# Optimization experiments

Measured on AMD Instinct MI355X. Metric: run time of the kernel, lower is better.

## Reference

```python
import jax, jax.numpy as jnp
import numpy as np

HEADS = 8
GROUPS = 32   # Group_cnt in the source
WIN = 16      # config.local_window_size


def _gn_nc(x, groups, eps):
    # group_norm on [N, C] (affine=False)
    N, C = x.shape
    xg = x.reshape(N, groups, C // groups)
    m = xg.mean(axis=2, keepdims=True)
    v = xg.var(axis=2, keepdims=True)
    return ((xg - m) / jnp.sqrt(v + eps)).reshape(N, C)


def _gn_nchw(x, groups, eps):
    # group_norm on [B, C, H, W] (affine=False)
    B, C, H, W = x.shape
    xg = x.reshape(B, groups, C // groups, H, W)
    m = xg.mean(axis=(2, 3, 4), keepdims=True)
    v = xg.var(axis=(2, 3, 4), keepdims=True)
    return ((xg - m) / jnp.sqrt(v + eps)).reshape(B, C, H, W)


def _conv3x3(x, w, b=None):
    y = jax.lax.conv_general_dilated(x, w, (1, 1), 'SAME',
                                     dimension_numbers=('NCHW', 'OIHW', 'NCHW'))
    return y if b is None else y + b[None, :, None, None]


def _forward(x, temb, conv1_w, conv1_b, conv2_w, g_diff, g_res, g2, g3,
             qkv2_w, qkv2_b, out2_w, qkv3_w, qkv3_b, out3_w,
             lsa_qkv_w, lsa_out_w):
    # ---- Residual_Block (layer1) ----
    h = _gn_nchw(x, GROUPS, 1e-6)
    h = _conv3x3(h, conv1_w, conv1_b)
    h = h + g_diff * temb[:, :, None, None]      # gate_diffusion (ReZero-style gate)
    h = jax.nn.silu(h)
    h = _gn_nchw(h, GROUPS, 1e-6)
    h = _conv3x3(h, conv2_w)
    h = _gn_nchw(h, GROUPS, 1e-6)
    x = x + g_res * h                            # gate_residual

    B, C, Fq, T = x.shape
    Dh = C // HEADS
    scale = 1.0 / jnp.sqrt(jnp.float32(Dh))      # (F/heads)**0.5 divisor

    # ---- SelfAttention over frequency axis (layer2): batch B*T, seq Fq ----
    xf = x.transpose(0, 3, 2, 1).reshape(B * T, Fq, C)
    qkv = xf @ qkv2_w + qkv2_b                   # [B*T, Fq, 3C]
    q, k, v = [t.reshape(B * T, Fq, HEADS, Dh) for t in jnp.split(qkv, 3, axis=-1)]
    p = jax.nn.softmax(jnp.einsum('bLhf,blhf->bLlh', q, k) * scale, axis=2)
    y = jnp.einsum('blhf,bLlh->bLhf', v, p).reshape(B * T, Fq, C) @ out2_w
    y = _gn_nc(y.reshape(-1, C), GROUPS, 1e-5).reshape(B * T, Fq, C)
    xf = xf + g2 * y                             # gate2

    # ---- GlobalAttention over time axis (layer3): batch B*Fq, seq T ----
    xt = xf.reshape(B, T, Fq, C).transpose(0, 2, 1, 3).reshape(B * Fq, T, C)
    qkv = xt @ qkv3_w + qkv3_b
    q, k, v = [t.reshape(B * Fq, T, HEADS, Dh) for t in jnp.split(qkv, 3, axis=-1)]
    p = jax.nn.softmax(jnp.einsum('bhf,blhf->blh', q.mean(axis=1), k) * scale, axis=1)
    y = jnp.einsum('blhf,blh->bhf', v, p).reshape(B * Fq, C) @ out3_w
    y = _gn_nc(y, GROUPS, 1e-5).reshape(B * Fq, 1, C)
    xt = xt + g3 * y                             # gate3, broadcast over T
    x = xt.reshape(B, Fq, T, C).transpose(0, 3, 1, 2)

    # ---- LSA_block (layer4): pre-norm local windowed attention along T, residual ----
    h = _gn_nchw(x, GROUPS, 1e-5)
    h = h.transpose(0, 2, 3, 1).reshape(B * Fq, T, C)
    nw = T // WIN
    qkv = (h @ lsa_qkv_w).reshape(B * Fq, nw, WIN, 3 * C)
    q, k, v = [t.reshape(B * Fq, nw, WIN, HEADS, Dh) for t in jnp.split(qkv, 3, axis=-1)]
    p = jax.nn.softmax(jnp.einsum('nwqhd,nwkhd->nwqkh', q, k) * scale, axis=3)
    o = jnp.einsum('nwqkh,nwkhd->nwqhd', p, v).reshape(B * Fq, T, C) @ lsa_out_w
    return x + o.reshape(B, Fq, T, C).transpose(0, 3, 1, 2)


def setup_inputs() -> dict:
    key = jax.random.key(0)
    ks = jax.random.split(key, 10)
    B, C, Fq, T = 4, 256, 64, 256
    w = lambda k, s: jax.random.normal(k, s, dtype=jnp.float32) * 0.02
    return {
        'x': jax.random.normal(ks[0], (B, C, Fq, T), dtype=jnp.float32),
        'temb': jax.random.normal(ks[1], (B, C), dtype=jnp.float32),
        'conv1_w': w(ks[2], (C, C, 3, 3)),
        'conv1_b': jnp.zeros((C,), jnp.float32),
        'conv2_w': w(ks[3], (C, C, 3, 3)),
        'g_diff': jnp.full((1,), 0.5, jnp.float32),
        'g_res': jnp.full((1,), 0.5, jnp.float32),
        'g2': jnp.full((1,), 0.5, jnp.float32),
        'g3': jnp.full((1,), 0.5, jnp.float32),
        'qkv2_w': w(ks[4], (C, 3 * C)),
        'qkv2_b': jnp.zeros((3 * C,), jnp.float32),
        'out2_w': w(ks[5], (C, C)),
        'qkv3_w': w(ks[6], (C, 3 * C)),
        'qkv3_b': jnp.zeros((3 * C,), jnp.float32),
        'out3_w': w(ks[7], (C, C)),
        'lsa_qkv_w': w(ks[8], (C, 3 * C)),
        'lsa_out_w': w(ks[9], (C, C)),
    }


def reference(x, temb, conv1_w, conv1_b, conv2_w, g_diff, g_res, g2, g3,
              qkv2_w, qkv2_b, out2_w, qkv3_w, qkv3_b, out3_w,
              lsa_qkv_w, lsa_out_w):
    return _forward(x, temb, conv1_w, conv1_b, conv2_w, g_diff, g_res, g2, g3,
                    qkv2_w, qkv2_b, out2_w, qkv3_w, qkv3_b, out3_w,
                    lsa_qkv_w, lsa_out_w)
```

## Files before the change

### kernel.cpp

```cpp
#include <hip/hip_runtime.h>

#define NN 16777216
#define CC 256
#define FF 64
#define TT 256

typedef short v8s __attribute__((ext_vector_type(8)));
typedef float v4f __attribute__((ext_vector_type(4)));

__device__ __forceinline__ unsigned short f2bf(float f) {
  unsigned u = __float_as_uint(f);
  u += 0x7fff + ((u >> 16) & 1);
  return (unsigned short)(u >> 16);
}
__device__ __forceinline__ float bf2f(unsigned short h) {
  return __uint_as_float(((unsigned)h) << 16);
}
__device__ __forceinline__ unsigned packbf2(float a, float b) {
  return (unsigned)f2bf(a) | ((unsigned)f2bf(b) << 16);
}
__device__ __forceinline__ void unpack8(uint4 u, float* d) {
  d[0] = __uint_as_float(u.x << 16); d[1] = __uint_as_float(u.x & 0xffff0000u);
  d[2] = __uint_as_float(u.y << 16); d[3] = __uint_as_float(u.y & 0xffff0000u);
  d[4] = __uint_as_float(u.z << 16); d[5] = __uint_as_float(u.z & 0xffff0000u);
  d[6] = __uint_as_float(u.w << 16); d[7] = __uint_as_float(u.w & 0xffff0000u);
}

__device__ __forceinline__ void blockReduce2(float& a, float& b, float* sbuf) {
  #pragma unroll
  for (int off = 32; off > 0; off >>= 1) {
    a += __shfl_down(a, off, 64);
    b += __shfl_down(b, off, 64);
  }
  int w = threadIdx.x >> 6;
  if ((threadIdx.x & 63) == 0) { sbuf[w] = a; sbuf[4 + w] = b; }
  __syncthreads();
  if (threadIdx.x == 0) {
    a = sbuf[0] + sbuf[1] + sbuf[2] + sbuf[3];
    b = sbuf[4] + sbuf[5] + sbuf[6] + sbuf[7];
  }
}

__global__ void prep_all_k(const float* __restrict__ c1w, const float* __restrict__ c2w,
    const float* __restrict__ q2w, const float* __restrict__ o2w, const float* __restrict__ q3w,
    const float* __restrict__ lqw, const float* __restrict__ low,
    unsigned short* __restrict__ WB1, unsigned short* __restrict__ WB2,
    unsigned short* __restrict__ Q2T, unsigned short* __restrict__ O2T,
    unsigned short* __restrict__ Q3T, unsigned short* __restrict__ LQT,
    unsigned short* __restrict__ LOT, float* __restrict__ stats) {
  long s = (long)blockIdx.x * 256 + threadIdx.x;
  if (s < 1024) { stats[s] = 0.f; return; }
  s -= 1024;
  if (s < 589824) {
    int co = (int)(s / 2304), r = (int)(s % 2304);
    int ci = r / 9, tap = r % 9;
    WB1[(tap * 256 + co) * 256 + ci] = f2bf(c1w[s]);
    return;
  }
  s -= 589824;
  if (s < 589824) {
    int co = (int)(s / 2304), r = (int)(s % 2304);
    int ci = r / 9, tap = r % 9;
    WB2[(tap * 256 + co) * 256 + ci] = f2bf(c2w[s]);
    return;
  }
  s -= 589824;
  if (s < 196608) { int k = (int)(s / 768), n = (int)(s % 768); Q2T[n * 256 + k] = f2bf(q2w[s]); return; }
  s -= 196608;
  if (s < 65536)  { int k = (int)(s / 256), n = (int)(s % 256); O2T[n * 256 + k] = f2bf(o2w[s]); return; }
  s -= 65536;
  if (s < 196608) { int k = (int)(s / 768), n = (int)(s % 768); Q3T[n * 256 + k] = f2bf(q3w[s]); return; }
  s -= 196608;
  if (s < 196608) { int k = (int)(s / 768), n = (int)(s % 768); LQT[n * 256 + k] = f2bf(lqw[s]); return; }
  s -= 196608;
  if (s < 65536)  { int k = (int)(s / 256), n = (int)(s % 256); LOT[n * 256 + k] = f2bf(low[s]); return; }
}

__global__ __launch_bounds__(256) void gn_stats_contig(const float* __restrict__ src, float* __restrict__ stats) {
  __shared__ float sbuf[8];
  int grp = blockIdx.x >> 3, chunk = blockIdx.x & 7;
  const float4* p = (const float4*)src + grp * 32768 + chunk * 4096;
  float s = 0.f, ss = 0.f;
  for (int i = threadIdx.x; i < 4096; i += 256) {
    float4 v = p[i];
    s += v.x + v.y + v.z + v.w;
    ss += v.x * v.x + v.y * v.y + v.z * v.z + v.w * v.w;
  }
  blockReduce2(s, ss, sbuf);
  if (threadIdx.x == 0) { atomicAdd(&stats[grp], s); atomicAdd(&stats[128 + grp], ss); }
}

__global__ __launch_bounds__(256) void gn_apply_tr_k(const float* __restrict__ src,
    const float* __restrict__ stats, unsigned short* __restrict__ XC, float eps) {
  __shared__ float sT[32][33];
  int bx = blockIdx.x;
  int r = bx >> 6;
  int c0 = ((bx >> 3) & 7) * 32;
  int t0 = (bx & 7) * 32;
  int b = r >> 6, f = r & 63;
  int tl = threadIdx.x & 31, tr = threadIdx.x >> 5;
  #pragma unroll
  for (int i = 0; i < 4; ++i) {
    int c = c0 + tr + i * 8;
    int grp = b * 32 + (c >> 3);
    float mean = stats[grp] * (1.f / 131072.f);
    float var = stats[128 + grp] * (1.f / 131072.f) - mean * mean;
    float rv = rsqrtf(var + eps);
    float v = src[((b * 256 + c) * 64 + f) * 256 + t0 + tl];
    sT[tr + i * 8][tl] = (v - mean) * rv;
  }
  __syncthreads();
  #pragma unroll
  for (int i = 0; i < 4; ++i) {
    int t = t0 + tr + i * 8;
    XC[(((size_t)(b * 64 + f)) * 256 + t) * 256 + c0 + tl] = f2bf(sT[tl][tr + i * 8]);
  }
}

__global__ __launch_bounds__(256) void gn_tr_resid_k(const float* __restrict__ h,
    const float* __restrict__ x, const float* __restrict__ stats,
    const float* __restrict__ gate, float* __restrict__ XF, float eps) {
  __shared__ float sT[32][33];
  int bx = blockIdx.x;
  int r = bx >> 6;
  int c0 = ((bx >> 3) & 7) * 32;
  int t0 = (bx & 7) * 32;
  int b = r >> 6, f = r & 63;
  int tl = threadIdx.x & 31, tr = threadIdx.x >> 5;
  float g = gate[0];
  #pragma unroll
  for (int i = 0; i < 4; ++i) {
    int c = c0 + tr + i * 8;
    int grp = b * 32 + (c >> 3);
    float mean = stats[grp] * (1.f / 131072.f);
    float var = stats[128 + grp] * (1.f / 131072.f) - mean * mean;
    float rv = rsqrtf(var + eps);
    int idx = ((b * 256 + c) * 64 + f) * 256 + t0 + tl;
    sT[tr + i * 8][tl] = x[idx] + g * (h[idx] - mean) * rv;
  }
  __syncthreads();
  #pragma unroll
  for (int i = 0; i < 4; ++i) {
    int t = t0 + tr + i * 8;
    XF[(((size_t)(b * 256 + t)) * 64 + f) * 256 + c0 + tl] = sT[tl][tr + i * 8];
  }
}

__global__ __launch_bounds__(256, 4) void conv3x3_mfma_k(const unsigned short* __restrict__ XC,
    const unsigned short* __restrict__ wb, const float* __restrict__ bias,
    const float* __restrict__ temb, const float* __restrict__ gd,
    float* __restrict__ out, float* __restrict__ ostats, int mode) {
  __shared__ __align__(16) unsigned short sIn[258][40];
  __shared__ __align__(16) unsigned short sW[3][64][40];
  int bid0 = blockIdx.y * 64 + blockIdx.x;
  int nb = (bid0 & 7) * 128 + (bid0 >> 3);
  int f  = nb & 63;
  int yy = nb >> 6;
  int b  = yy >> 2;
  int co0 = (yy & 3) * 64;
  int tid = threadIdx.x;
  int wave = tid >> 6, lane = tid & 63;
  int lm = lane & 15, quad = lane >> 4;
  int w64 = wave * 64;
  v4f acc[4][4];
  #pragma unroll
  for (int i = 0; i < 4; ++i)
    #pragma unroll
    for (int j = 0; j < 4; ++j) acc[i][j] = (v4f)(0.f);

  for (int ci0 = 0; ci0 < 256; ci0 += 32) {
    for (int df = 0; df < 3; ++df) {
      __syncthreads();
      for (int s = tid; s < 1032; s += 256) {
        int tl = s >> 2, part = s & 3;
        int fi = f + df - 1, tg = tl - 1;
        uint4 val = make_uint4(0, 0, 0, 0);
        if (fi >= 0 && fi < 64 && tg >= 0 && tg < 256)
          val = *(const uint4*)&XC[(((size_t)(b * 64 + fi)) * 256 + tg) * 256 + ci0 + part * 8];
        *(uint4*)&sIn[tl][part * 8] = val;
      }
      for (int s = tid; s < 768; s += 256) {
        int tap3 = s >> 8, r = s & 255;
        int co = r >> 2, part = r & 3;
        *(uint4*)&sW[tap3][co][part * 8] =
            *(const uint4*)&wb[((size_t)((df * 3 + tap3) * 256) + co0 + co) * 256 + ci0 + part * 8];
      }
      __syncthreads();
      #pragma unroll
      for (int dt = 0; dt < 3; ++dt) {
        v8s A[4];
        #pragma unroll
        for (int mt = 0; mt < 4; ++mt)
          A[mt] = *(const v8s*)&sIn[w64 + mt * 16 + lm + dt][quad * 8];
        #pragma unroll
        for (int nt = 0; nt < 4; ++nt) {
          v8s B = *(const v8s*)&sW[dt][nt * 16 + lm][quad * 8];
          #pragma unroll
          for (int mt = 0; mt < 4; ++mt)
            acc[mt][nt] = __builtin_amdgcn_mfma_f32_16x16x32_bf16(A[mt], B, acc[mt][nt], 0, 0, 0);
        }
      }
    }
  }
  __syncthreads();
  float* sStat = (float*)sIn;
  float gdv = mode ? gd[0] : 0.f;
  float sch, qch;
  #pragma unroll
  for (int nt = 0; nt < 4; ++nt) {
    int co = co0 + nt * 16 + lm;
    float bb = 0.f;
    if (mode) bb = bias[co] + gdv * temb[b * 256 + co];
    sch = 0.f; qch = 0.f;
    #pragma unroll
    for (int mt = 0; mt < 4; ++mt) {
      int t = w64 + mt * 16 + quad * 4;
      float v0 = acc[mt][nt][0] + bb, v1 = acc[mt][nt][1] + bb;
      float v2 = acc[mt][nt][2] + bb, v3 = acc[mt][nt][3] + bb;
      if (mode) {
        v0 = v0 / (1.f + expf(-v0)); v1 = v1 / (1.f + expf(-v1));
        v2 = v2 / (1.f + expf(-v2)); v3 = v3 / (1.f + expf(-v3));
      }
      float4 o; o.x = v0; o.y = v1; o.z = v2; o.w = v3;
      *(float4*)&out[(((size_t)b * 256 + co) * 64 + f) * 256 + t] = o;
      sch += v0 + v1 + v2 + v3;
      qch += v0 * v0 + v1 * v1 + v2 * v2 + v3 * v3;
    }
    sch += __shfl_xor(sch, 16); qch += __shfl_xor(qch, 16);
    sch += __shfl_xor(sch, 32); qch += __shfl_xor(qch, 32);
    if (quad == 0) {
      sStat[((wave * 4 + nt) * 16 + lm) * 2]     = sch;
      sStat[((wave * 4 + nt) * 16 + lm) * 2 + 1] = qch;
    }
  }
  __syncthreads();
  if (tid < 64) {
    int c = tid;
    int nt = c >> 4, lmm = c & 15;
    float s = 0.f, q = 0.f;
    #pragma unroll
    for (int w = 0; w < 4; ++w) {
      s += sStat[((w * 4 + nt) * 16 + lmm) * 2];
      q += sStat[((w * 4 + nt) * 16 + lmm) * 2 + 1];
    }
    s += __shfl_xor(s, 1); q += __shfl_xor(q, 1);
    s += __shfl_xor(s, 2); q += __shfl_xor(q, 2);
    s += __shfl_xor(s, 4); q += __shfl_xor(q, 4);
    if ((c & 7) == 0) {
      int g = (co0 + c) >> 3;
      atomicAdd(&ostats[b * 32 + g], s);
      atomicAdd(&ostats[128 + b * 32 + g], q);
    }
  }
}

__global__ __launch_bounds__(256) void gemm_af32_k(const float* __restrict__ A, int lda,
    const unsigned short* __restrict__ BT, const float* __restrict__ bias,
    unsigned short* __restrict__ Cb, int ldc,
    const float* __restrict__ gstats, int growbase, float eps) {
  __shared__ __align__(16) unsigned short sA[128][40];
  __shared__ __align__(16) unsigned short sB[128][40];
  int nbx = gridDim.x;
  int nwg = nbx * gridDim.y;
  int bid0 = blockIdx.y * nbx + blockIdx.x;
  int nb = (bid0 & 7) * (nwg >> 3) + (bid0 >> 3);
  int n0 = (nb % nbx) * 128, m0 = (nb / nbx) * 128;
  int tid = threadIdx.x;
  int wave = tid >> 6, lane = tid & 63;
  int wm = wave >> 1, wn = wave & 1;
  int lm = lane & 15, quad = lane >> 4;
  v4f acc[4][4];
  #pragma unroll
  for (int i = 0; i < 4; ++i)
    #pragma unroll
    for (int j = 0; j < 4; ++j) acc[i][j] = (v4f)(0.f);

  for (int k0 = 0; k0 < 256; k0 += 32) {
    __syncthreads();
    #pragma unroll
    for (int i = 0; i < 4; ++i) {
      int s = tid + i * 256;
      int row = s >> 3, k4 = s & 7;
      float4 av = *(const float4*)&A[(size_t)(m0 + row) * lda + k0 + k4 * 4];
      if (gstats) {
        int grp = ((growbase + m0 + row) >> 14) * 32 + ((k0 + k4 * 4) >> 3);
        float mean = gstats[grp] * (1.f / 131072.f);
        float var = gstats[128 + grp] * (1.f / 131072.f) - mean * mean;
        float rr = rsqrtf(var + eps);
        av.x = (av.x - mean) * rr; av.y = (av.y - mean) * rr;
        av.z = (av.z - mean) * rr; av.w = (av.w - mean) * rr;
      }
      *(uint2*)&sA[row][k4 * 4] = make_uint2(packbf2(av.x, av.y), packbf2(av.z, av.w));
    }
    #pragma unroll
    for (int i = 0; i < 2; ++i) {
      int s = tid + i * 256;
      int n = s >> 2, part = s & 3;
      *(uint4*)&sB[n][part * 8] = *(const uint4*)&BT[(size_t)(n0 + n) * 256 + k0 + part * 8];
    }
    __syncthreads();
    v8s Af[4];
    #pragma unroll
    for (int mt = 0; mt < 4; ++mt)
      Af[mt] = *(const v8s*)&sA[wm * 64 + mt * 16 + lm][quad * 8];
    #pragma unroll
    for (int nt = 0; nt < 4; ++nt) {
      v8s Bf = *(const v8s*)&sB[wn * 64 + nt * 16 + lm][quad * 8];
      #pragma unroll
      for (int mt = 0; mt < 4; ++mt)
        acc[mt][nt] = __builtin_amdgcn_mfma_f32_16x16x32_bf16(Af[mt], Bf, acc[mt][nt], 0, 0, 0);
    }
  }
  #pragma unroll
  for (int nt = 0; nt < 4; ++nt) {
    int col = n0 + wn * 64 + nt * 16 + lm;
    float bb = bias ? bias[col] : 0.f;
    #pragma unroll
    for (int mt = 0; mt < 4; ++mt) {
      int row = m0 + wm * 64 + mt * 16 + quad * 4;
      #pragma unroll
      for (int r = 0; r < 4; ++r)
        Cb[(size_t)(row + r) * ldc + col] = f2bf(acc[mt][nt][r] + bb);
    }
  }
}

__global__ __launch_bounds__(256) void gemm_abf16_k(const unsigned short* __restrict__ A, int lda,
    const unsigned short* __restrict__ BT, float* __restrict__ xf,
    unsigned short* __restrict__ Cb, int ldc, const float* __restrict__ gate) {
  __shared__ __align__(16) unsigned short sA[128][40];
  __shared__ __align__(16) unsigned short sB[128][40];
  int nbx = gridDim.x;
  int nwg = nbx * gridDim.y;
  int bid0 = blockIdx.y * nbx + blockIdx.x;
  int nb = (bid0 & 7) * (nwg >> 3) + (bid0 >> 3);
  int n0 = (nb % nbx) * 128, m0 = (nb / nbx) * 128;
  int tid = threadIdx.x;
  int wave = tid >> 6, lane = tid & 63;
  int wm = wave >> 1, wn = wave & 1;
  int lm = lane & 15, quad = lane >> 4;
  v4f acc[4][4];
  #pragma unroll
  for (int i = 0; i < 4; ++i)
    #pragma unroll
    for (int j = 0; j < 4; ++j) acc[i][j] = (v4f)(0.f);

  for (int k0 = 0; k0 < 256; k0 += 32) {
    __syncthreads();
    #pragma unroll
    for (int i = 0; i < 2; ++i) {
      int s = tid + i * 256;
      int row = s >> 2, part = s & 3;
      *(uint4*)&sA[row][part * 8] = *(const uint4*)&A[(size_t)(m0 + row) * lda + k0 + part * 8];
      *(uint4*)&sB[row][part * 8] = *(const uint4*)&BT[(size_t)(n0 + row) * 256 + k0 + part * 8];
    }
    __syncthreads();
    v8s Af[4];
    #pragma unroll
    for (int mt = 0; mt < 4; ++mt)
      Af[mt] = *(const v8s*)&sA[wm * 64 + mt * 16 + lm][quad * 8];
    #pragma unroll
    for (int nt = 0; nt < 4; ++nt) {
      v8s Bf = *(const v8s*)&sB[wn * 64 + nt * 16 + lm][quad * 8];
      #pragma unroll
      for (int mt = 0; mt < 4; ++mt)
        acc[mt][nt] = __builtin_amdgcn_mfma_f32_16x16x32_bf16(Af[mt], Bf, acc[mt][nt], 0, 0, 0);
    }
  }
  if (xf) {
    float g = gate[0];
    #pragma unroll
    for (int mt = 0; mt < 4; ++mt) {
      int rowb = m0 + wm * 64 + mt * 16 + quad * 4;
      #pragma unroll
      for (int r = 0; r < 4; ++r) {
        #pragma unroll
        for (int nt = 0; nt < 4; ++nt) {
          float v = acc[mt][nt][r];
          float s = v, q = v * v;
          s += __shfl_xor(s, 1); q += __shfl_xor(q, 1);
          s += __shfl_xor(s, 2); q += __shfl_xor(q, 2);
          s += __shfl_xor(s, 4); q += __shfl_xor(q, 4);
          float m = s * 0.125f;
          float var = q * 0.125f - m * m;
          float norm = (v - m) * rsqrtf(var + 1e-5f);
          int col = n0 + wn * 64 + nt * 16 + lm;
          size_t idx = (size_t)(rowb + r) * 256 + col;
          xf[idx] += g * norm;
        }
      }
    }
  } else {
    #pragma unroll
    for (int nt = 0; nt < 4; ++nt) {
      int col = n0 + wn * 64 + nt * 16 + lm;
      #pragma unroll
      for (int mt = 0; mt < 4; ++mt) {
        int row = m0 + wm * 64 + mt * 16 + quad * 4;
        #pragma unroll
        for (int r = 0; r < 4; ++r)
          Cb[(size_t)(row + r) * ldc + col] = f2bf(acc[mt][nt][r]);
      }
    }
  }
}

__global__ __launch_bounds__(256) void gemm_k(const float* __restrict__ A, int lda,
    const float* __restrict__ Bm, int N, const float* __restrict__ bias,
    float* __restrict__ Cm, int ldc, int gn) {
  __shared__ __align__(16) float sA[16][64];
  __shared__ __align__(16) float sB[16][64];
  int n0 = blockIdx.x * 64, m0 = blockIdx.y * 64;
  int tid = threadIdx.x;
  int tx = tid & 15, ty = tid >> 4;
  int arow = m0 + (tid >> 2), acol = (tid & 3) * 4;
  int brow = tid >> 4, bcol = (tid & 15) * 4;
  float acc[4][4] = {};
  for (int k0 = 0; k0 < 256; k0 += 16) {
    __syncthreads();
    float4 av = *(const float4*)&A[(size_t)arow * lda + k0 + acol];
    sA[acol + 0][tid >> 2] = av.x;
    sA[acol + 1][tid >> 2] = av.y;
    sA[acol + 2][tid >> 2] = av.z;
    sA[acol + 3][tid >> 2] = av.w;
    *(float4*)&sB[brow][bcol] = *(const float4*)&Bm[(k0 + brow) * N + n0 + bcol];
    __syncthreads();
    #pragma unroll
    for (int kk = 0; kk < 16; ++kk) {
      float4 a = *(const float4*)&sA[kk][ty * 4];
      float4 b = *(const float4*)&sB[kk][tx * 4];
      float aa[4] = {a.x, a.y, a.z, a.w};
      float bb[4] = {b.x, b.y, b.z, b.w};
      #pragma unroll
      for (int i = 0; i < 4; ++i)
        #pragma unroll
        for (int j = 0; j < 4; ++j)
          acc[i][j] += aa[i] * bb[j];
    }
  }
  #pragma unroll
  for (int i = 0; i < 4; ++i) {
    float m = 0.f, rv = 1.f;
    if (gn) {
      float s = acc[i][0] + acc[i][1] + acc[i][2] + acc[i][3];
      float q = acc[i][0] * acc[i][0] + acc[i][1] * acc[i][1]
              + acc[i][2] * acc[i][2] + acc[i][3] * acc[i][3];
      s += __shfl_xor(s, 1); q += __shfl_xor(q, 1);
      m = s * 0.125f;
      float var = q * 0.125f - m * m;
      rv = rsqrtf(var + 1e-5f);
    }
    #pragma unroll
    for (int j = 0; j < 4; ++j) {
      int n = n0 + tx * 4 + j;
      float v = acc[i][j];
      if (gn) v = (v - m) * rv;
      else if (bias) v += bias[n];
      Cm[(size_t)(m0 + ty * 4 + i) * ldc + n] = v;
    }
  }
}

__global__ __launch_bounds__(256) void xf_to_xt_k(const float* __restrict__ XF, float* __restrict__ XT) {
  int rowid = blockIdx.x * 4 + (threadIdx.x >> 6);
  int lane = threadIdx.x & 63;
  int b = rowid >> 14, f = (rowid >> 8) & 63, t = rowid & 255;
  int src = ((b * TT + t) * FF + f) * CC + lane * 4;
  int dst = rowid * CC + lane * 4;
  *(float4*)&XT[dst] = *(const float4*)&XF[src];
}

__global__ __launch_bounds__(256) void final_out_k(const float* __restrict__ XT,
    const unsigned short* __restrict__ O2b, float* __restrict__ out, int rbase) {
  __shared__ float sT[32][33];
  int bx = blockIdx.x;
  int rl = bx >> 6;
  int t0 = ((bx >> 3) & 7) * 32;
  int c0 = (bx & 7) * 32;
  int rg = rbase + rl;
  int b = rg >> 6, f = rg & 63;
  int tc = threadIdx.x & 31, tr = threadIdx.x >> 5;
  #pragma unroll
  for (int i = 0; i < 4; ++i) {
    int t = t0 + tr + i * 8;
    sT[tr + i * 8][tc] = XT[(size_t)rg * 65536 + t * 256 + c0 + tc]
                       + bf2f(O2b[(size_t)rl * 65536 + t * 256 + c0 + tc]);
  }
  __syncthreads();
  #pragma unroll
  for (int i = 0; i < 4; ++i) {
    int c = c0 + tr + i * 8;
    out[((b * CC + c) * FF + f) * TT + t0 + tc] = sT[tc][tr + i * 8];
  }
}

__global__ __launch_bounds__(256) void attn2_mfma_k(unsigned short* __restrict__ Q) {
  __shared__ __align__(16) unsigned short sP[4][64][72];
  __shared__ __align__(16) unsigned short sVt[4][32][72];
  int bt = blockIdx.x;
  int tid = threadIdx.x;
  int wave = tid >> 6, lane = tid & 63;
  int lm = lane & 15, quad = lane >> 4;
  const float scale = 0.17677669529663687f;
  size_t rowbase = (size_t)bt * 64;
  unsigned short (*P)[72] = sP[wave];
  unsigned short (*Vt)[72] = sVt[wave];
  #pragma unroll
  for (int hh = 0; hh < 2; ++hh) {
    int h = wave * 2 + hh;
    int hoff = h * 32;
    v8s Af[4], Bf[4];
    #pragma unroll
    for (int mt = 0; mt < 4; ++mt)
      Af[mt] = *(const v8s*)&Q[(rowbase + mt * 16 + lm) * 768 + hoff + quad * 8];
    #pragma unroll
    for (int nt = 0; nt < 4; ++nt)
      Bf[nt] = *(const v8s*)&Q[(rowbase + nt * 16 + lm) * 768 + 256 + hoff + quad * 8];
    v4f S[4][4];
    #pragma unroll
    for (int mt = 0; mt < 4; ++mt)
      #pragma unroll
      for (int nt = 0; nt < 4; ++nt)
        S[mt][nt] = __builtin_amdgcn_mfma_f32_16x16x32_bf16(Af[mt], Bf[nt], (v4f)(0.f), 0, 0, 0);
    #pragma unroll
    for (int part = 0; part < 4; ++part) {
      uint4 u = *(const uint4*)&Q[(rowbase + lane) * 768 + 512 + hoff + part * 8];
      unsigned short* up = (unsigned short*)&u;
      #pragma unroll
      for (int j = 0; j < 8; ++j) Vt[part * 8 + j][lane] = up[j];
    }
    float inv[4][4];
    #pragma unroll
    for (int mt = 0; mt < 4; ++mt) {
      #pragma unroll
      for (int r = 0; r < 4; ++r) {
        float v0 = S[mt][0][r] * scale, v1 = S[mt][1][r] * scale;
        float v2 = S[mt][2][r] * scale, v3 = S[mt][3][r] * scale;
        float mx = fmaxf(fmaxf(v0, v1), fmaxf(v2, v3));
        mx = fmaxf(mx, __shfl_xor(mx, 1));
        mx = fmaxf(mx, __shfl_xor(mx, 2));
        mx = fmaxf(mx, __shfl_xor(mx, 4));
        mx = fmaxf(mx, __shfl_xor(mx, 8));
        float e0 = __expf(v0 - mx), e1 = __expf(v1 - mx);
        float e2 = __expf(v2 - mx), e3 = __expf(v3 - mx);
        float sm = e0 + e1 + e2 + e3;
        sm += __shfl_xor(sm, 1);
        sm += __shfl_xor(sm, 2);
        sm += __shfl_xor(sm, 4);
        sm += __shfl_xor(sm, 8);
        inv[mt][r] = 1.f / sm;
        int row = mt * 16 + quad * 4 + r;
        P[row][lm]      = f2bf(e0);
        P[row][16 + lm] = f2bf(e1);
        P[row][32 + lm] = f2bf(e2);
        P[row][48 + lm] = f2bf(e3);
      }
    }
    v8s Ap[4][2], Bv[2][2];
    #pragma unroll
    for (int mt = 0; mt < 4; ++mt)
      #pragma unroll
      for (int kc = 0; kc < 2; ++kc)
        Ap[mt][kc] = *(const v8s*)&P[mt * 16 + lm][kc * 32 + quad * 8];
    #pragma unroll
    for (int nd = 0; nd < 2; ++nd)
      #pragma unroll
      for (int kc = 0; kc < 2; ++kc)
        Bv[nd][kc] = *(const v8s*)&Vt[nd * 16 + lm][kc * 32 + quad * 8];
    #pragma unroll
    for (int mt = 0; mt < 4; ++mt) {
      #pragma unroll
      for (int nd = 0; nd < 2; ++nd) {
        v4f O = (v4f)(0.f);
        O = __builtin_amdgcn_mfma_f32_16x16x32_bf16(Ap[mt][0], Bv[nd][0], O, 0, 0, 0);
        O = __builtin_amdgcn_mfma_f32_16x16x32_bf16(Ap[mt][1], Bv[nd][1], O, 0, 0, 0);
        #pragma unroll
        for (int r = 0; r < 4; ++r)
          P[mt * 16 + quad * 4 + r][nd * 16 + lm] = f2bf(O[r] * inv[mt][r]);
      }
    }
    #pragma unroll
    for (int part = 0; part < 4; ++part) {
      uint4 u = *(const uint4*)&P[lane][part * 8];
      *(uint4*)&Q[(rowbase + lane) * 768 + hoff + part * 8] = u;
    }
  }
}

__global__ __launch_bounds__(256) void attn3_k(const unsigned short* __restrict__ Q3,
                                               float* __restrict__ y3, int bf_base) {
  __shared__ float sQp[64][33];
  __shared__ float sqm[32];
  __shared__ float sp[256];
  __shared__ float sred[256];
  int bfl = blockIdx.x >> 3, h = blockIdx.x & 7;
  int tid = threadIdx.x;
  int tq = tid >> 2, c4 = tid & 3;
  int d8 = c4 * 8;
  const float scale = 0.17677669529663687f;
  size_t rowbase = (size_t)bfl * 256;
  {
    float a[8] = {};
    #pragma unroll
    for (int i = 0; i < 4; ++i) {
      int t = i * 64 + tq;
      float v[8];
      unpack8(*(const uint4*)&Q3[(rowbase + t) * 768 + h * 32 + d8], v);
      #pragma unroll
      for (int j = 0; j < 8; ++j) a[j] += v[j];
    }
    #pragma unroll
    for (int j = 0; j < 8; ++j) sQp[tq][d8 + j] = a[j];
  }
  __syncthreads();
  if (tid < 32) {
    float m = 0.f;
    for (int g = 0; g < 64; ++g) m += sQp[g][tid];
    sqm[tid] = m * (1.f / 256.f);
  }
  __syncthreads();
  {
    float dot = 0.f;
    #pragma unroll
    for (int p = 0; p < 4; ++p) {
      float v[8];
      unpack8(*(const uint4*)&Q3[(rowbase + tid) * 768 + 256 + h * 32 + p * 8], v);
      #pragma unroll
      for (int j = 0; j < 8; ++j) dot += sqm[p * 8 + j] * v[j];
    }
    sp[tid] = dot * scale;
    sred[tid] = sp[tid];
  }
  __syncthreads();
  for (int st = 128; st > 0; st >>= 1) { if (tid < st) sred[tid] = fmaxf(sred[tid], sred[tid + st]); __syncthreads(); }
  float mx = sred[0];
  __syncthreads();
  float e = expf(sp[tid] - mx);
  sred[tid] = e;
  __syncthreads();
  for (int st = 128; st > 0; st >>= 1) { if (tid < st) sred[tid] += sred[tid + st]; __syncthreads(); }
  float rinv = 1.f / sred[0];
  sp[tid] = e * rinv;
  __syncthreads();
  {
    float a[8] = {};
    #pragma unroll
    for (int i = 0; i < 4; ++i) {
      int t = i * 64 + tq;
      float w = sp[t];
      float v[8];
      unpack8(*(const uint4*)&Q3[(rowbase + t) * 768 + 512 + h * 32 + d8], v);
      #pragma unroll
      for (int j = 0; j < 8; ++j) a[j] += w * v[j];
    }
    #pragma unroll
    for (int j = 0; j < 8; ++j) sQp[tq][d8 + j] = a[j];
  }
  __syncthreads();
  if (tid < 32) {
    float o = 0.f;
    for (int g = 0; g < 64; ++g) o += sQp[g][tid];
    y3[(size_t)(bf_base + bfl) * 256 + h * 32 + tid] = o;
  }
}

__global__ __launch_bounds__(256) void lsa_attn_k(unsigned short* __restrict__ Q4) {
  __shared__ __align__(16) float sX[16][772];
  __shared__ float sS[8][16][17];
  __shared__ float sInv[8][16];
  int bfl = blockIdx.x >> 4, w = blockIdx.x & 15;
  int tid = threadIdx.x;
  size_t rb = ((size_t)(bfl * 256 + w * 16)) * 768;
  for (int s = tid; s < 1536; s += 256) {
    int t = s / 96, c8 = (s - t * 96) * 8;
    unpack8(*(const uint4*)&Q4[rb + t * 768 + c8], &sX[t][c8]);
  }
  __syncthreads();
  const float scale = 0.17677669529663687f;
  #pragma unroll
  for (int rep = 0; rep < 8; ++rep) {
    int idx = tid + rep * 256;
    int h = idx >> 8, q = (idx >> 4) & 15, k = idx & 15;
    float dot = 0.f;
    const float* qp = &sX[q][h * 32];
    const float* kp = &sX[k][256 + h * 32];
    for (int d = 0; d < 32; ++d) dot += qp[d] * kp[d];
    sS[h][q][k] = dot * scale;
  }
  __syncthreads();
  if (tid < 128) {
    int h = tid >> 4, q = tid & 15;
    float mx = -1e30f;
    for (int k = 0; k < 16; ++k) mx = fmaxf(mx, sS[h][q][k]);
    float sum = 0.f;
    for (int k = 0; k < 16; ++k) { float e = expf(sS[h][q][k] - mx); sS[h][q][k] = e; sum += e; }
    sInv[h][q] = 1.f / sum;
  }
  __syncthreads();
  #pragma unroll
  for (int rep = 0; rep < 8; ++rep) {
    int idx = tid + rep * 256;
    int t = idx >> 7, c2 = (idx & 127) * 2;
    int h = c2 >> 5;
    float a0 = 0.f, a1 = 0.f;
    for (int k = 0; k < 16; ++k) {
      float p = sS[h][t][k];
      a0 += p * sX[k][512 + c2];
      a1 += p * sX[k][512 + c2 + 1];
    }
    float riv = sInv[h][t];
    *(unsigned*)&Q4[rb + t * 768 + c2] = packbf2(a0 * riv, a1 * riv);
  }
}

__global__ __launch_bounds__(256) void bcast_add_k(float* __restrict__ XT, const float* __restrict__ y3n,
                                                   const float* __restrict__ gate) {
  int i4 = blockIdx.x * 256 + threadIdx.x;
  int flat = i4 * 4;
  int r = flat >> 16, c = flat & 255;
  float g = gate[0];
  float4 v = ((float4*)XT)[i4];
  float4 a = *(const float4*)&y3n[r * 256 + c];
  v.x += g * a.x; v.y += g * a.y; v.z += g * a.z; v.w += g * a.w;
  ((float4*)XT)[i4] = v;
}

__global__ __launch_bounds__(256) void gn_stats_xt_k(const float* __restrict__ X, float* __restrict__ stats) {
  __shared__ float sbuf[8];
  int bx = blockIdx.x;
  int b = bx >> 11, g = (bx >> 6) & 31, f = bx & 63;
  size_t base = (size_t)(b * 64 + f) * 65536 + g * 8;
  float s = 0.f, ss = 0.f;
  for (int i = threadIdx.x; i < 2048; i += 256) {
    int t = i >> 3, c = i & 7;
    float v = X[base + t * 256 + c];
    s += v; ss += v * v;
  }
  blockReduce2(s, ss, sbuf);
  if (threadIdx.x == 0) { atomicAdd(&stats[b * 32 + g], s); atomicAdd(&stats[128 + b * 32 + g], ss); }
}

extern "C" void kernel_launch(void* const* d_in, const int* in_sizes, int n_in,
                              void* d_out, int out_size, void* d_ws, size_t ws_size,
                              hipStream_t stream) {
  (void)in_sizes; (void)n_in; (void)out_size;
  const float* x        = (const float*)d_in[0];
  const float* temb     = (const float*)d_in[1];
  const float* conv1_w  = (const float*)d_in[2];
  const float* conv1_b  = (const float*)d_in[3];
  const float* conv2_w  = (const float*)d_in[4];
  const float* g_diff   = (const float*)d_in[5];
  const float* g_res    = (const float*)d_in[6];
  const float* g2       = (const float*)d_in[7];
  const float* g3       = (const float*)d_in[8];
  const float* qkv2_w   = (const float*)d_in[9];
  const float* qkv2_b   = (const float*)d_in[10];
  const float* out2_w   = (const float*)d_in[11];
  const float* qkv3_w   = (const float*)d_in[12];
  const float* qkv3_b   = (const float*)d_in[13];
  const float* out3_w   = (const float*)d_in[14];
  const float* lsa_qkv_w = (const float*)d_in[15];
  const float* lsa_out_w = (const float*)d_in[16];
  float* out = (float*)d_out;
  float* ws = (float*)d_ws;

  int NCHv = 4;
  {
    auto need = [](int nch) -> size_t {
      size_t rows = 65536 / nch;
      size_t uslots = rows * 512;
      if (uslots < 8388608) uslots = 8388608;
      return 4ull * ((size_t)NN + uslots + 950272 + 198000);
    };
    if (ws_size >= need(1)) NCHv = 1;
    else if (ws_size >= need(2)) NCHv = 2;
  }
  const size_t rows = 65536 / NCHv;

  float* W = ws;
  float* U = ws + (size_t)NN;
  unsigned short* XC  = (unsigned short*)U;
  unsigned short* QB  = (unsigned short*)U;
  unsigned short* O2B = (unsigned short*)(U + rows * 384);
  size_t uslots = rows * 512; if (uslots < 8388608) uslots = 8388608;
  float* WREG = U + uslots;
  unsigned short* WB1   = (unsigned short*)WREG;
  unsigned short* WB2   = WB1 + 589824;
  unsigned short* QKV2T = WB2 + 589824;
  unsigned short* OUT2T = QKV2T + 196608;
  unsigned short* QKV3T = OUT2T + 65536;
  unsigned short* LSAQT = QKV3T + 196608;
  unsigned short* LSAOT = LSAQT + 196608;
  float* Y3    = WREG + 950272;
  float* Y3O   = Y3 + 65536;
  float* Y3N   = Y3O + 65536;
  float* STATS = Y3N + 65536;
  float* ST0 = STATS, *ST1 = STATS + 256, *ST2 = STATS + 512, *ST3 = STATS + 768;
  float* D = out;

  dim3 b256(256);
  prep_all_k<<<7428, b256, 0, stream>>>(conv1_w, conv2_w, qkv2_w, out2_w, qkv3_w,
                                        lsa_qkv_w, lsa_out_w,
                                        WB1, WB2, QKV2T, OUT2T, QKV3T, LSAQT, LSAOT, STATS);

  gn_stats_contig<<<1024, b256, 0, stream>>>(x, ST0);
  gn_apply_tr_k<<<16384, b256, 0, stream>>>(x, ST0, XC, 1e-6f);
  conv3x3_mfma_k<<<dim3(64, 16), b256, 0, stream>>>(XC, WB1, conv1_b, temb, g_diff, W, ST1, 1);
  gn_apply_tr_k<<<16384, b256, 0, stream>>>(W, ST1, XC, 1e-6f);
  conv3x3_mfma_k<<<dim3(64, 16), b256, 0, stream>>>(XC, WB2, nullptr, nullptr, nullptr, W, ST2, 0);
  gn_tr_resid_k<<<16384, b256, 0, stream>>>(W, x, ST2, g_res, D, 1e-6f);

  for (int c = 0; c < NCHv; ++c) {
    float* XFr = D + (size_t)c * rows * 256;
    gemm_af32_k<<<dim3(6, rows / 128), b256, 0, stream>>>(XFr, 256, QKV2T, qkv2_b, QB, 768, nullptr, 0, 0.f);
    attn2_mfma_k<<<rows / 64, b256, 0, stream>>>(QB);
    gemm_abf16_k<<<dim3(2, rows / 128), b256, 0, stream>>>(QB, 768, OUT2T, XFr, nullptr, 256, g2);
  }

  xf_to_xt_k<<<16384, b256, 0, stream>>>(D, W);
  for (int c = 0; c < NCHv; ++c) {
    const float* XTr = W + (size_t)c * rows * 256;
    gemm_af32_k<<<dim3(6, rows / 128), b256, 0, stream>>>(XTr, 256, QKV3T, qkv3_b, QB, 768, nullptr, 0, 0.f);
    attn3_k<<<(rows / 256) * 8, b256, 0, stream>>>(QB, Y3, c * (int)(rows / 256));
  }
  gemm_k<<<dim3(4, 4), b256, 0, stream>>>(Y3, 256, out3_w, 256, nullptr, Y3N, 256, 1);
  bcast_add_k<<<16384, b256, 0, stream>>>(W, Y3N, g3);

  gn_stats_xt_k<<<8192, b256, 0, stream>>>(W, ST3);
  for (int c = 0; c < NCHv; ++c) {
    const float* XTr = W + (size_t)c * rows * 256;
    gemm_af32_k<<<dim3(6, rows / 128), b256, 0, stream>>>(XTr, 256, LSAQT, nullptr, QB, 768,
                                                          ST3, (int)(c * rows), 1e-5f);
    lsa_attn_k<<<(rows / 256) * 16, b256, 0, stream>>>(QB);
    gemm_abf16_k<<<dim3(2, rows / 128), b256, 0, stream>>>(QB, 768, LSAOT, nullptr, O2B, 256, nullptr);
    final_out_k<<<(rows / 256) * 64, b256, 0, stream>>>(W, O2B, out, c * (int)(rows / 256));
  }
}
```

Baseline: 1.104 ms.

## Fuse xf-to-xt transpose into out2 GEMM epilogue and drop block swizzling

The out2 projection GEMM epilogue now writes the gated residual result straight into the time-major XT layout, instead of updating XF in place and running a separate transpose kernel. This removes one full read and write pass over the 16M-element activation and one kernel launch. The scattered row writes in the epilogue may be less coalesced. The XCD-aware block index swizzle is also removed from the conv and GEMM kernels, which changes L2 locality across chiplets.

```diff
diff --git a/kernel.cpp b/kernel.cpp
--- a/kernel.cpp
+++ b/kernel.cpp
@@ -152,12 +152,9 @@
     float* __restrict__ out, float* __restrict__ ostats, int mode) {
   __shared__ __align__(16) unsigned short sIn[258][40];
   __shared__ __align__(16) unsigned short sW[3][64][40];
-  int bid0 = blockIdx.y * 64 + blockIdx.x;
-  int nb = (bid0 & 7) * 128 + (bid0 >> 3);
-  int f  = nb & 63;
-  int yy = nb >> 6;
-  int b  = yy >> 2;
-  int co0 = (yy & 3) * 64;
+  int f  = blockIdx.x;
+  int b  = blockIdx.y >> 2;
+  int co0 = (blockIdx.y & 3) * 64;
   int tid = threadIdx.x;
   int wave = tid >> 6, lane = tid & 63;
   int lm = lane & 15, quad = lane >> 4;
@@ -260,11 +257,7 @@
     const float* __restrict__ gstats, int growbase, float eps) {
   __shared__ __align__(16) unsigned short sA[128][40];
   __shared__ __align__(16) unsigned short sB[128][40];
-  int nbx = gridDim.x;
-  int nwg = nbx * gridDim.y;
-  int bid0 = blockIdx.y * nbx + blockIdx.x;
-  int nb = (bid0 & 7) * (nwg >> 3) + (bid0 >> 3);
-  int n0 = (nb % nbx) * 128, m0 = (nb / nbx) * 128;
+  int n0 = blockIdx.x * 128, m0 = blockIdx.y * 128;
   int tid = threadIdx.x;
   int wave = tid >> 6, lane = tid & 63;
   int wm = wave >> 1, wn = wave & 1;
@@ -326,15 +319,12 @@
 }
 
 __global__ __launch_bounds__(256) void gemm_abf16_k(const unsigned short* __restrict__ A, int lda,
-    const unsigned short* __restrict__ BT, float* __restrict__ xf,
+    const unsigned short* __restrict__ BT,
+    const float* __restrict__ xfin, float* __restrict__ xtout, int rowbase,
     unsigned short* __restrict__ Cb, int ldc, const float* __restrict__ gate) {
   __shared__ __align__(16) unsigned short sA[128][40];
   __shared__ __align__(16) unsigned short sB[128][40];
-  int nbx = gridDim.x;
-  int nwg = nbx * gridDim.y;
-  int bid0 = blockIdx.y * nbx + blockIdx.x;
-  int nb = (bid0 & 7) * (nwg >> 3) + (bid0 >> 3);
-  int n0 = (nb % nbx) * 128, m0 = (nb / nbx) * 128;
+  int n0 = blockIdx.x * 128, m0 = blockIdx.y * 128;
   int tid = threadIdx.x;
   int wave = tid >> 6, lane = tid & 63;
   int wm = wave >> 1, wn = wave & 1;
@@ -367,13 +357,17 @@
         acc[mt][nt] = __builtin_amdgcn_mfma_f32_16x16x32_bf16(Af[mt], Bf, acc[mt][nt], 0, 0, 0);
     }
   }
-  if (xf) {
+  if (xtout) {
     float g = gate[0];
     #pragma unroll
     for (int mt = 0; mt < 4; ++mt) {
       int rowb = m0 + wm * 64 + mt * 16 + quad * 4;
       #pragma unroll
       for (int r = 0; r < 4; ++r) {
+        int rowl = rowb + r;
+        int rowg = rowbase + rowl;
+        int b = rowg >> 14, t = (rowg >> 6) & 255, fq = rowg & 63;
+        size_t xtrow = (size_t)((b * 64 + fq) * 256 + t) * 256;
         #pragma unroll
         for (int nt = 0; nt < 4; ++nt) {
           float v = acc[mt][nt][r];
@@ -385,8 +379,7 @@
           float var = q * 0.125f - m * m;
           float norm = (v - m) * rsqrtf(var + 1e-5f);
           int col = n0 + wn * 64 + nt * 16 + lm;
-          size_t idx = (size_t)(rowb + r) * 256 + col;
-          xf[idx] += g * norm;
+          xtout[xtrow + col] = xfin[(size_t)rowl * 256 + col] + g * norm;
         }
       }
     }
@@ -459,15 +452,6 @@
       Cm[(size_t)(m0 + ty * 4 + i) * ldc + n] = v;
     }
   }
-}
-
-__global__ __launch_bounds__(256) void xf_to_xt_k(const float* __restrict__ XF, float* __restrict__ XT) {
-  int rowid = blockIdx.x * 4 + (threadIdx.x >> 6);
-  int lane = threadIdx.x & 63;
-  int b = rowid >> 14, f = (rowid >> 8) & 63, t = rowid & 255;
-  int src = ((b * TT + t) * FF + f) * CC + lane * 4;
-  int dst = rowid * CC + lane * 4;
-  *(float4*)&XT[dst] = *(const float4*)&XF[src];
 }
 
 __global__ __launch_bounds__(256) void final_out_k(const float* __restrict__ XT,
@@ -814,10 +798,11 @@
     float* XFr = D + (size_t)c * rows * 256;
     gemm_af32_k<<<dim3(6, rows / 128), b256, 0, stream>>>(XFr, 256, QKV2T, qkv2_b, QB, 768, nullptr, 0, 0.f);
     attn2_mfma_k<<<rows / 64, b256, 0, stream>>>(QB);
-    gemm_abf16_k<<<dim3(2, rows / 128), b256, 0, stream>>>(QB, 768, OUT2T, XFr, nullptr, 256, g2);
-  }
-
-  xf_to_xt_k<<<16384, b256, 0, stream>>>(D, W);
+    gemm_abf16_k<<<dim3(2, rows / 128), b256, 0, stream>>>(QB, 768, OUT2T,
+                                                           XFr, W, (int)(c * rows),
+                                                           nullptr, 256, g2);
+  }
+
   for (int c = 0; c < NCHv; ++c) {
     const float* XTr = W + (size_t)c * rows * 256;
     gemm_af32_k<<<dim3(6, rows / 128), b256, 0, stream>>>(XTr, 256, QKV3T, qkv3_b, QB, 768, nullptr, 0, 0.f);
@@ -832,7 +817,9 @@
     gemm_af32_k<<<dim3(6, rows / 128), b256, 0, stream>>>(XTr, 256, LSAQT, nullptr, QB, 768,
                                                           ST3, (int)(c * rows), 1e-5f);
     lsa_attn_k<<<(rows / 256) * 16, b256, 0, stream>>>(QB);
-    gemm_abf16_k<<<dim3(2, rows / 128), b256, 0, stream>>>(QB, 768, LSAOT, nullptr, O2B, 256, nullptr);
+    gemm_abf16_k<<<dim3(2, rows / 128), b256, 0, stream>>>(QB, 768, LSAOT,
+                                                           nullptr, nullptr, 0,
+                                                           O2B, 256, nullptr);
     final_out_k<<<(rows / 256) * 64, b256, 0, stream>>>(W, O2B, out, c * (int)(rows / 256));
   }
 }
```

Result: faster. 1.060 ms (-4.0%).
